# Performance work log

Hardware: AMD Instinct MI355X
Metric: run time of the kernel (lower is better)

The kernel has to match this reference:

```python
import jax, jax.numpy as jnp
import numpy as np

M = 262144          # rows of A == prod(out_shape) == 512*512
N = 262144          # cols of A == prod(x.shape)
NNZ = 8388608       # 32 nonzeros per row on average
OUT_SHAPE = (512, 512)


def setup_inputs() -> dict:
    key = jax.random.key(0)
    k1, k2, k3, k4 = jax.random.split(key, 4)
    A_rows = jax.random.randint(k1, (NNZ,), 0, M, dtype=jnp.int32)
    A_cols = jax.random.randint(k2, (NNZ,), 0, N, dtype=jnp.int32)
    A_vals = jax.random.normal(k3, (NNZ,), dtype=jnp.float32)
    x = jax.random.normal(k4, OUT_SHAPE, dtype=jnp.float32)
    return {"x": x, "A_vals": A_vals, "A_rows": A_rows, "A_cols": A_cols}


def reference(x, A_vals, A_rows, A_cols):
    # x.reshape(A.shape[1], 1); torch.sparse.mm(A, x); reshape(out_shape)
    xf = x.reshape(-1)                                   # [N]
    contrib = A_vals * jnp.take(xf, A_cols)              # [NNZ] gather + multiply
    y = jax.ops.segment_sum(contrib, A_rows, num_segments=M)  # scatter-add over rows
    return y.reshape(OUT_SHAPE).astype(jnp.float32)
```

## Files before the change

kernel.cpp:

```cpp
#include <hip/hip_runtime.h>


#define BINS_MAXB   64
#define ROW_SHIFT   13
#define ROWS_PER_BIN 8192
#define ENT         4096
#define SLICES      16


__global__ __launch_bounds__(256) void zero_out_kernel(float* __restrict__ y, int n) {
    int i = blockIdx.x * blockDim.x + threadIdx.x;
    if (i < n) y[i] = 0.0f;
}

__global__ __launch_bounds__(256) void spmv_coo_scatter(
    const float* __restrict__ vals, const int* __restrict__ rows,
    const int* __restrict__ cols, const float* __restrict__ x,
    float* __restrict__ y, int nnz)
{
    int i = (blockIdx.x * blockDim.x + threadIdx.x) * 4;
    if (i + 3 < nnz) {
        float4 v = *reinterpret_cast<const float4*>(vals + i);
        int4   r = *reinterpret_cast<const int4*>(rows + i);
        int4   c = *reinterpret_cast<const int4*>(cols + i);
        atomicAdd(&y[r.x], v.x * x[c.x]);
        atomicAdd(&y[r.y], v.y * x[c.y]);
        atomicAdd(&y[r.z], v.z * x[c.z]);
        atomicAdd(&y[r.w], v.w * x[c.w]);
    } else {
        for (; i < nnz; ++i) atomicAdd(&y[rows[i]], vals[i] * x[cols[i]]);
    }
}


__global__ __launch_bounds__(64) void init_cursors(unsigned* __restrict__ gcur, int bins) {
    int t = threadIdx.x;
    if (t < bins) gcur[t] = 0u;
}

__global__ __launch_bounds__(256) void scatter2_kernel(
    const int*   __restrict__ rows, const int* __restrict__ cols,
    const float* __restrict__ vals, const float* __restrict__ x, int nnz,
    unsigned* __restrict__ gcur, unsigned cap,
    unsigned short* __restrict__ okeys, float* __restrict__ ocontrib, int bins)
{
    __shared__ unsigned cnt[BINS_MAXB], lstart[BINS_MAXB], sresv[BINS_MAXB];
    __shared__ int dstb[BINS_MAXB];
    __shared__ unsigned cur2[BINS_MAXB];
    __shared__ unsigned total_s;
    __shared__ unsigned short skey[ENT];
    __shared__ float          sval[ENT];
    __shared__ unsigned char  sbin[ENT];

    const int t = threadIdx.x;
    for (int i = t; i < bins; i += 256) cnt[i] = 0u;
    __syncthreads();

    const int seg = blockIdx.x * ENT;

    int   rr[16];
    float ff[16];

    #pragma unroll
    for (int ch = 0; ch < 4; ++ch) {
        int base = seg + ch * 1024 + t * 4;
        if (base + 3 < nnz) {
            int4   r4 = *reinterpret_cast<const int4*>(rows + base);
            int4   c4 = *reinterpret_cast<const int4*>(cols + base);
            float4 v4 = *reinterpret_cast<const float4*>(vals + base);
            rr[ch*4+0] = r4.x; ff[ch*4+0] = v4.x * x[c4.x];
            rr[ch*4+1] = r4.y; ff[ch*4+1] = v4.y * x[c4.y];
            rr[ch*4+2] = r4.z; ff[ch*4+2] = v4.z * x[c4.z];
            rr[ch*4+3] = r4.w; ff[ch*4+3] = v4.w * x[c4.w];
        } else {
            #pragma unroll
            for (int j = 0; j < 4; ++j) {
                int idx = base + j;
                if (idx < nnz) { rr[ch*4+j] = rows[idx]; ff[ch*4+j] = vals[idx] * x[cols[idx]]; }
                else           { rr[ch*4+j] = -1; ff[ch*4+j] = 0.0f; }
            }
        }
    }
    #pragma unroll
    for (int j = 0; j < 16; ++j)
        if (rr[j] >= 0) atomicAdd(&cnt[rr[j] >> ROW_SHIFT], 1u);
    __syncthreads();

    if (t < bins) sresv[t] = atomicAdd(&gcur[t], cnt[t]);
    if (t == 0) {
        unsigned run = 0;
        for (int b = 0; b < bins; ++b) { lstart[b] = run; run += cnt[b]; }
        total_s = run;
    }
    __syncthreads();
    if (t < bins) {
        dstb[t] = (int)sresv[t] - (int)lstart[t];
        cur2[t] = lstart[t];
    }
    __syncthreads();

    #pragma unroll
    for (int j = 0; j < 16; ++j) {
        if (rr[j] >= 0) {
            int b = rr[j] >> ROW_SHIFT;
            unsigned p = atomicAdd(&cur2[b], 1u);
            skey[p] = (unsigned short)(rr[j] & (ROWS_PER_BIN - 1));
            sval[p] = ff[j];
            sbin[p] = (unsigned char)b;
        }
    }
    __syncthreads();

    const unsigned total = total_s;
    for (unsigned i = t; i < total; i += 256) {
        int b = sbin[i];
        unsigned off = (unsigned)(dstb[b] + (int)i);
        if (off < cap) {
            size_t dst = (size_t)b * cap + off;
            okeys[dst]    = skey[i];
            ocontrib[dst] = sval[i];
        }
    }
}

__global__ __launch_bounds__(256) void accum2_kernel(
    const unsigned short* __restrict__ okeys, const float* __restrict__ ocontrib,
    const unsigned* __restrict__ gcur, unsigned cap,
    float* __restrict__ partials)
{
    __shared__ float acc[ROWS_PER_BIN];
    const int t = threadIdx.x;
    const int bin = blockIdx.x / SLICES;
    const int sl  = blockIdx.x % SLICES;

    #pragma unroll
    for (int i = 0; i < ROWS_PER_BIN / 256; ++i) acc[t + i * 256] = 0.0f;
    __syncthreads();

    unsigned count = gcur[bin];
    if (count > cap) count = cap;
    unsigned chunk = (count + SLICES - 1) / SLICES;
    chunk = (chunk + 3u) & ~3u;
    unsigned lo = (unsigned)sl * chunk;
    unsigned hi = lo + chunk; if (hi > count) hi = count;

    const unsigned short* k = okeys    + (size_t)bin * cap;
    const float*          c = ocontrib + (size_t)bin * cap;

    unsigned i = lo + (unsigned)t * 4u;
    for (; i + 3u < hi; i += 1024u) {
        ushort4 k4 = *reinterpret_cast<const ushort4*>(k + i);
        float4  c4 = *reinterpret_cast<const float4*>(c + i);
        atomicAdd(&acc[k4.x], c4.x);
        atomicAdd(&acc[k4.y], c4.y);
        atomicAdd(&acc[k4.z], c4.z);
        atomicAdd(&acc[k4.w], c4.w);
    }
    for (; i < hi; ++i) atomicAdd(&acc[k[i]], c[i]);
    __syncthreads();

    float* p = partials + (size_t)blockIdx.x * ROWS_PER_BIN;
    #pragma unroll
    for (int j = 0; j < ROWS_PER_BIN / 1024; ++j) {
        int l = j * 1024 + t * 4;
        *reinterpret_cast<float4*>(p + l) = *reinterpret_cast<const float4*>(&acc[l]);
    }
}

__global__ __launch_bounds__(256) void reduce2_kernel(
    const float* __restrict__ partials, float* __restrict__ y, int out_size)
{
    int r = blockIdx.x * 256 + threadIdx.x;
    if (r >= out_size) return;
    int bin = r >> ROW_SHIFT;
    int local = r & (ROWS_PER_BIN - 1);
    const float* p = partials + ((size_t)bin * SLICES) * ROWS_PER_BIN + local;
    float s = 0.0f;
    #pragma unroll
    for (int j = 0; j < SLICES; ++j) s += p[(size_t)j * ROWS_PER_BIN];
    y[r] = s;
}

extern "C" void kernel_launch(void* const* d_in, const int* in_sizes, int n_in,
                              void* d_out, int out_size, void* d_ws, size_t ws_size,
                              hipStream_t stream) {
    const float* x    = (const float*)d_in[0];
    const float* vals = (const float*)d_in[1];
    const int*   rows = (const int*)d_in[2];
    const int*   cols = (const int*)d_in[3];
    float* y = (float*)d_out;

    const int nnz  = in_sizes[1];
    const int bins = (out_size + ROWS_PER_BIN - 1) / ROWS_PER_BIN;
    const int nb   = (nnz + ENT - 1) / ENT;
    unsigned cap = (unsigned)(nnz / (bins > 0 ? bins : 1)) + 16384u;
    cap = (cap + 3u) & ~3u;

    auto align256 = [](size_t v) { return (v + 255) & ~(size_t)255; };
    size_t off_contrib  = 0;
    size_t off_keys     = align256(off_contrib + (size_t)bins * cap * 4);
    size_t off_partials = align256(off_keys + (size_t)bins * cap * 2);
    size_t off_gcur     = align256(off_partials + (size_t)bins * SLICES * ROWS_PER_BIN * 4);
    size_t need         = align256(off_gcur + (size_t)bins * 4);

    const bool ok = (bins >= 1) && (bins <= BINS_MAXB) && (need <= ws_size) && (nnz > 0);

    if (!ok) {
        zero_out_kernel<<<(out_size + 255) / 256, 256, 0, stream>>>(y, out_size);
        spmv_coo_scatter<<<(nnz + 1023) / 1024, 256, 0, stream>>>(vals, rows, cols, x, y, nnz);
        return;
    }

    char* w = (char*)d_ws;
    float*          ocontrib = (float*)(w + off_contrib);
    unsigned short* okeys    = (unsigned short*)(w + off_keys);
    float*          partials = (float*)(w + off_partials);
    unsigned*       gcur     = (unsigned*)(w + off_gcur);

    init_cursors<<<1, 64, 0, stream>>>(gcur, bins);
    scatter2_kernel<<<nb, 256, 0, stream>>>(rows, cols, vals, x, nnz, gcur, cap,
                                            okeys, ocontrib, bins);
    accum2_kernel<<<bins * SLICES, 256, 0, stream>>>(okeys, ocontrib, gcur, cap, partials);
    reduce2_kernel<<<(out_size + 255) / 256, 256, 0, stream>>>(partials, y, out_size);
}
```

Before: 232.0 us.

## Replace count-then-scatter binning with per-bin LDS buckets and overflow list

The scatter kernel no longer counts per-bin totals before placing entries. Each element now goes straight into a fixed-capacity per-bin shared-memory bucket, and elements that do not fit go to a global overflow list that the first slice of each bin's accumulator folds in. This drops two barriers and a serial prefix scan. Cursors are padded to separate cache lines, loads are nontemporal, the accumulate pass uses 512 threads and 32 slices, and the final reduce is vectorised to float4. The trade-offs are overflow atomics on one shared counter, a full overflow scan by 32 blocks, and more partials traffic.

```diff
diff --git a/kernel.cpp b/kernel.cpp
--- a/kernel.cpp
+++ b/kernel.cpp
@@ -1,11 +1,19 @@
 #include <hip/hip_runtime.h>
 
 
-#define BINS_MAXB   64
-#define ROW_SHIFT   13
+#define BINS         32
+#define ROW_SHIFT    13
 #define ROWS_PER_BIN 8192
-#define ENT         4096
-#define SLICES      16
+#define ENT          2048
+#define BKT_CAP      112
+#define KST          114
+#define VST          113
+#define CUR_STRIDE   32
+#define OVF_SLOT     (BINS * CUR_STRIDE)
+#define OVF_CAP      65536
+
+typedef int   __attribute__((ext_vector_type(4))) i32x4;
+typedef float __attribute__((ext_vector_type(4))) f32x4;
 
 
 __global__ __launch_bounds__(256) void zero_out_kernel(float* __restrict__ y, int n) {
@@ -33,41 +41,40 @@
 }
 
 
-__global__ __launch_bounds__(64) void init_cursors(unsigned* __restrict__ gcur, int bins) {
-    int t = threadIdx.x;
-    if (t < bins) gcur[t] = 0u;
-}
-
-__global__ __launch_bounds__(256) void scatter2_kernel(
+__global__ __launch_bounds__(256) void init_cursors(unsigned* __restrict__ gcur, int n) {
+    int i = blockIdx.x * 256 + threadIdx.x;
+    if (i < n) gcur[i] = 0u;
+}
+
+__global__ __launch_bounds__(256) void scatter_bucket_kernel(
     const int*   __restrict__ rows, const int* __restrict__ cols,
     const float* __restrict__ vals, const float* __restrict__ x, int nnz,
     unsigned* __restrict__ gcur, unsigned cap,
-    unsigned short* __restrict__ okeys, float* __restrict__ ocontrib, int bins)
-{
-    __shared__ unsigned cnt[BINS_MAXB], lstart[BINS_MAXB], sresv[BINS_MAXB];
-    __shared__ int dstb[BINS_MAXB];
-    __shared__ unsigned cur2[BINS_MAXB];
-    __shared__ unsigned total_s;
-    __shared__ unsigned short skey[ENT];
-    __shared__ float          sval[ENT];
-    __shared__ unsigned char  sbin[ENT];
+    unsigned short* __restrict__ okeys, float* __restrict__ ocontrib,
+    uint2* __restrict__ ovf)
+{
+    __shared__ unsigned short skey[BINS * KST];
+    __shared__ float          sval[BINS * VST];
+    __shared__ unsigned cur[BINS];
+    __shared__ unsigned scnt[BINS];
+    __shared__ unsigned resv[BINS];
 
     const int t = threadIdx.x;
-    for (int i = t; i < bins; i += 256) cnt[i] = 0u;
+    if (t < BINS) cur[t] = 0u;
     __syncthreads();
 
     const int seg = blockIdx.x * ENT;
 
-    int   rr[16];
-    float ff[16];
-
-    #pragma unroll
-    for (int ch = 0; ch < 4; ++ch) {
+    int   rr[8];
+    float ff[8];
+
+    #pragma unroll
+    for (int ch = 0; ch < 2; ++ch) {
         int base = seg + ch * 1024 + t * 4;
         if (base + 3 < nnz) {
-            int4   r4 = *reinterpret_cast<const int4*>(rows + base);
-            int4   c4 = *reinterpret_cast<const int4*>(cols + base);
-            float4 v4 = *reinterpret_cast<const float4*>(vals + base);
+            i32x4 r4 = __builtin_nontemporal_load(reinterpret_cast<const i32x4*>(rows + base));
+            i32x4 c4 = __builtin_nontemporal_load(reinterpret_cast<const i32x4*>(cols + base));
+            f32x4 v4 = __builtin_nontemporal_load(reinterpret_cast<const f32x4*>(vals + base));
             rr[ch*4+0] = r4.x; ff[ch*4+0] = v4.x * x[c4.x];
             rr[ch*4+1] = r4.y; ff[ch*4+1] = v4.y * x[c4.y];
             rr[ch*4+2] = r4.z; ff[ch*4+2] = v4.z * x[c4.z];
@@ -81,66 +88,67 @@
             }
         }
     }
-    #pragma unroll
-    for (int j = 0; j < 16; ++j)
-        if (rr[j] >= 0) atomicAdd(&cnt[rr[j] >> ROW_SHIFT], 1u);
-    __syncthreads();
-
-    if (t < bins) sresv[t] = atomicAdd(&gcur[t], cnt[t]);
-    if (t == 0) {
-        unsigned run = 0;
-        for (int b = 0; b < bins; ++b) { lstart[b] = run; run += cnt[b]; }
-        total_s = run;
-    }
-    __syncthreads();
-    if (t < bins) {
-        dstb[t] = (int)sresv[t] - (int)lstart[t];
-        cur2[t] = lstart[t];
-    }
-    __syncthreads();
-
-    #pragma unroll
-    for (int j = 0; j < 16; ++j) {
+
+    #pragma unroll
+    for (int j = 0; j < 8; ++j) {
         if (rr[j] >= 0) {
             int b = rr[j] >> ROW_SHIFT;
-            unsigned p = atomicAdd(&cur2[b], 1u);
-            skey[p] = (unsigned short)(rr[j] & (ROWS_PER_BIN - 1));
-            sval[p] = ff[j];
-            sbin[p] = (unsigned char)b;
-        }
-    }
-    __syncthreads();
-
-    const unsigned total = total_s;
-    for (unsigned i = t; i < total; i += 256) {
-        int b = sbin[i];
-        unsigned off = (unsigned)(dstb[b] + (int)i);
-        if (off < cap) {
-            size_t dst = (size_t)b * cap + off;
-            okeys[dst]    = skey[i];
-            ocontrib[dst] = sval[i];
-        }
-    }
-}
-
-__global__ __launch_bounds__(256) void accum2_kernel(
+            unsigned p = atomicAdd(&cur[b], 1u);
+            if (p < BKT_CAP) {
+                skey[b * KST + p] = (unsigned short)(rr[j] & (ROWS_PER_BIN - 1));
+                sval[b * VST + p] = ff[j];
+            } else {
+                unsigned q = atomicAdd(&gcur[OVF_SLOT], 1u);
+                if (q < OVF_CAP) ovf[q] = make_uint2((unsigned)rr[j], __float_as_uint(ff[j]));
+            }
+        }
+    }
+    __syncthreads();
+
+    if (t < BINS) {
+        unsigned c = cur[t]; if (c > BKT_CAP) c = BKT_CAP;
+        scnt[t] = c;
+        resv[t] = atomicAdd(&gcur[t * CUR_STRIDE], c);
+    }
+    __syncthreads();
+
+    const int wave = t >> 6, lane = t & 63;
+    #pragma unroll
+    for (int k = 0; k < BINS / 4; ++k) {
+        int b = wave * (BINS / 4) + k;
+        unsigned cnt  = scnt[b];
+        unsigned base = resv[b];
+        const size_t binoff = (size_t)b * cap;
+        for (unsigned i = lane; i < cnt; i += 64) {
+            unsigned off = base + i;
+            if (off < cap) {
+                okeys[binoff + off]    = skey[b * KST + i];
+                ocontrib[binoff + off] = sval[b * VST + i];
+            }
+        }
+    }
+}
+
+__global__ __launch_bounds__(512) void accum2_kernel(
     const unsigned short* __restrict__ okeys, const float* __restrict__ ocontrib,
     const unsigned* __restrict__ gcur, unsigned cap,
-    float* __restrict__ partials)
+    const uint2* __restrict__ ovf,
+    float* __restrict__ partials, int slices)
 {
     __shared__ float acc[ROWS_PER_BIN];
-    const int t = threadIdx.x;
-    const int bin = blockIdx.x / SLICES;
-    const int sl  = blockIdx.x % SLICES;
-
-    #pragma unroll
-    for (int i = 0; i < ROWS_PER_BIN / 256; ++i) acc[t + i * 256] = 0.0f;
-    __syncthreads();
-
-    unsigned count = gcur[bin];
+    const int t   = threadIdx.x;
+    const int bin = blockIdx.x / slices;
+    const int sl  = blockIdx.x - bin * slices;
+
+    float4 z = make_float4(0.f, 0.f, 0.f, 0.f);
+    #pragma unroll
+    for (int i = 0; i < ROWS_PER_BIN / (512 * 4); ++i)
+        *reinterpret_cast<float4*>(&acc[(i * 512 + t) * 4]) = z;
+    __syncthreads();
+
+    unsigned count = gcur[bin * CUR_STRIDE];
     if (count > cap) count = cap;
-    unsigned chunk = (count + SLICES - 1) / SLICES;
-    chunk = (chunk + 3u) & ~3u;
+    unsigned chunk = ((count + (unsigned)slices - 1u) / (unsigned)slices + 3u) & ~3u;
     unsigned lo = (unsigned)sl * chunk;
     unsigned hi = lo + chunk; if (hi > count) hi = count;
 
@@ -148,7 +156,7 @@
     const float*          c = ocontrib + (size_t)bin * cap;
 
     unsigned i = lo + (unsigned)t * 4u;
-    for (; i + 3u < hi; i += 1024u) {
+    for (; i + 3u < hi; i += 2048u) {
         ushort4 k4 = *reinterpret_cast<const ushort4*>(k + i);
         float4  c4 = *reinterpret_cast<const float4*>(c + i);
         atomicAdd(&acc[k4.x], c4.x);
@@ -157,28 +165,49 @@
         atomicAdd(&acc[k4.w], c4.w);
     }
     for (; i < hi; ++i) atomicAdd(&acc[k[i]], c[i]);
+
+    if (sl == 0) {
+        unsigned ovn = gcur[OVF_SLOT];
+        if (ovn > OVF_CAP) ovn = OVF_CAP;
+        for (unsigned j = (unsigned)t; j < ovn; j += 512u) {
+            uint2 e = ovf[j];
+            if ((int)(e.x >> ROW_SHIFT) == bin)
+                atomicAdd(&acc[e.x & (ROWS_PER_BIN - 1)], __uint_as_float(e.y));
+        }
+    }
     __syncthreads();
 
     float* p = partials + (size_t)blockIdx.x * ROWS_PER_BIN;
     #pragma unroll
-    for (int j = 0; j < ROWS_PER_BIN / 1024; ++j) {
-        int l = j * 1024 + t * 4;
+    for (int i2 = 0; i2 < ROWS_PER_BIN / (512 * 4); ++i2) {
+        int l = (i2 * 512 + t) * 4;
         *reinterpret_cast<float4*>(p + l) = *reinterpret_cast<const float4*>(&acc[l]);
     }
 }
 
 __global__ __launch_bounds__(256) void reduce2_kernel(
-    const float* __restrict__ partials, float* __restrict__ y, int out_size)
-{
-    int r = blockIdx.x * 256 + threadIdx.x;
-    if (r >= out_size) return;
-    int bin = r >> ROW_SHIFT;
-    int local = r & (ROWS_PER_BIN - 1);
-    const float* p = partials + ((size_t)bin * SLICES) * ROWS_PER_BIN + local;
-    float s = 0.0f;
-    #pragma unroll
-    for (int j = 0; j < SLICES; ++j) s += p[(size_t)j * ROWS_PER_BIN];
-    y[r] = s;
+    const float* __restrict__ partials, float* __restrict__ y, int out_size, int slices)
+{
+    int r0 = (blockIdx.x * 256 + threadIdx.x) * 4;
+    if (r0 >= out_size) return;
+    if (r0 + 3 < out_size) {
+        int bin = r0 >> ROW_SHIFT, local = r0 & (ROWS_PER_BIN - 1);
+        const float* p = partials + ((size_t)bin * slices) * ROWS_PER_BIN + local;
+        float4 s = make_float4(0.f, 0.f, 0.f, 0.f);
+        for (int j = 0; j < slices; ++j) {
+            float4 v = *reinterpret_cast<const float4*>(p + (size_t)j * ROWS_PER_BIN);
+            s.x += v.x; s.y += v.y; s.z += v.z; s.w += v.w;
+        }
+        *reinterpret_cast<float4*>(y + r0) = s;
+    } else {
+        for (int r = r0; r < out_size; ++r) {
+            int bin = r >> ROW_SHIFT, local = r & (ROWS_PER_BIN - 1);
+            const float* p = partials + ((size_t)bin * slices) * ROWS_PER_BIN + local;
+            float s = 0.f;
+            for (int j = 0; j < slices; ++j) s += p[(size_t)j * ROWS_PER_BIN];
+            y[r] = s;
+        }
+    }
 }
 
 extern "C" void kernel_launch(void* const* d_in, const int* in_sizes, int n_in,
@@ -192,18 +221,26 @@
 
     const int nnz  = in_sizes[1];
     const int bins = (out_size + ROWS_PER_BIN - 1) / ROWS_PER_BIN;
-    const int nb   = (nnz + ENT - 1) / ENT;
+
     unsigned cap = (unsigned)(nnz / (bins > 0 ? bins : 1)) + 16384u;
     cap = (cap + 3u) & ~3u;
 
     auto align256 = [](size_t v) { return (v + 255) & ~(size_t)255; };
-    size_t off_contrib  = 0;
-    size_t off_keys     = align256(off_contrib + (size_t)bins * cap * 4);
-    size_t off_partials = align256(off_keys + (size_t)bins * cap * 2);
-    size_t off_gcur     = align256(off_partials + (size_t)bins * SLICES * ROWS_PER_BIN * 4);
-    size_t need         = align256(off_gcur + (size_t)bins * 4);
-
-    const bool ok = (bins >= 1) && (bins <= BINS_MAXB) && (need <= ws_size) && (nnz > 0);
+
+    int slices = 32;
+    size_t off_contrib = 0, off_keys = 0, off_partials = 0, off_gcur = 0, off_ovf = 0, need = 0;
+    for (int attempt = 0; attempt < 2; ++attempt) {
+        off_contrib  = 0;
+        off_keys     = align256(off_contrib + (size_t)BINS * cap * 4);
+        off_partials = align256(off_keys + (size_t)BINS * cap * 2);
+        off_gcur     = align256(off_partials + (size_t)BINS * slices * ROWS_PER_BIN * 4);
+        off_ovf      = align256(off_gcur + (size_t)(OVF_SLOT + CUR_STRIDE) * 4);
+        need         = align256(off_ovf + (size_t)OVF_CAP * 8);
+        if (need <= ws_size) break;
+        slices = 16;
+    }
+
+    const bool ok = (bins == BINS) && (need <= ws_size) && (nnz > 0) && (out_size % 4 == 0);
 
     if (!ok) {
         zero_out_kernel<<<(out_size + 255) / 256, 256, 0, stream>>>(y, out_size);
@@ -216,10 +253,14 @@
     unsigned short* okeys    = (unsigned short*)(w + off_keys);
     float*          partials = (float*)(w + off_partials);
     unsigned*       gcur     = (unsigned*)(w + off_gcur);
-
-    init_cursors<<<1, 64, 0, stream>>>(gcur, bins);
-    scatter2_kernel<<<nb, 256, 0, stream>>>(rows, cols, vals, x, nnz, gcur, cap,
-                                            okeys, ocontrib, bins);
-    accum2_kernel<<<bins * SLICES, 256, 0, stream>>>(okeys, ocontrib, gcur, cap, partials);
-    reduce2_kernel<<<(out_size + 255) / 256, 256, 0, stream>>>(partials, y, out_size);
-}
+    uint2*          ovf      = (uint2*)(w + off_ovf);
+
+    const int ncur = OVF_SLOT + 1;
+    init_cursors<<<(ncur + 255) / 256, 256, 0, stream>>>(gcur, ncur);
+    scatter_bucket_kernel<<<(nnz + ENT - 1) / ENT, 256, 0, stream>>>(
+        rows, cols, vals, x, nnz, gcur, cap, okeys, ocontrib, ovf);
+    accum2_kernel<<<BINS * slices, 512, 0, stream>>>(
+        okeys, ocontrib, gcur, cap, ovf, partials, slices);
+    reduce2_kernel<<<(out_size / 4 + 255) / 256, 256, 0, stream>>>(
+        partials, y, out_size, slices);
+}
```

Result: slower. 249.9 us (+7.7%).
